# Performance work log

Measured on AMD Instinct MI355X. Metric: run time of the kernel, lower is better.

The kernel has to match this reference:

```python
import jax, jax.numpy as jnp
import numpy as np

B, T, C = 4, 2048, 2048
H, S = 32, 64
LN_EPS = 1e-5


def _layer_norm(x, w, b):
    mu = jnp.mean(x, axis=-1, keepdims=True)
    var = jnp.mean((x - mu) ** 2, axis=-1, keepdims=True)
    return (x - mu) / jnp.sqrt(var + LN_EPS) * w + b


def setup_inputs() -> dict:
    key = jax.random.key(0)
    ks = jax.random.split(key, 8)
    sc = 1.0 / np.sqrt(C)
    sc4 = 1.0 / np.sqrt(4 * C)
    return {
        "x": jax.random.normal(ks[0], (B, T, C), jnp.float32),
        "time_decay": jnp.full((H, S), -5.0, jnp.float32),
        "time_first": jnp.zeros((H, S), jnp.float32),
        "Wk": jax.random.normal(ks[1], (C, C), jnp.float32) * sc,
        "Wv": jax.random.normal(ks[2], (C, C), jnp.float32) * sc,
        "Wr": jax.random.normal(ks[3], (C, C), jnp.float32) * sc,
        "Wo": jax.random.normal(ks[4], (C, C), jnp.float32) * sc,
        "Wfk": jax.random.normal(ks[5], (C, 4 * C), jnp.float32) * sc,
        "Wfv": jax.random.normal(ks[6], (4 * C, C), jnp.float32) * sc4,
        "ln1_w": jnp.ones((C,), jnp.float32),
        "ln1_b": jnp.zeros((C,), jnp.float32),
        "ln2_w": jnp.ones((C,), jnp.float32),
        "ln2_b": jnp.zeros((C,), jnp.float32),
    }


def reference(x, time_decay, time_first, Wk, Wv, Wr, Wo, Wfk, Wfv,
              ln1_w, ln1_b, ln2_w, ln2_b):
    b, t, c = x.shape
    h, s = time_decay.shape
    xl = _layer_norm(x, ln1_w, ln1_b)
    k = (xl @ Wk).reshape(b, t, h, s)  # [B,T,H,S]
    v = (xl @ Wv).reshape(b, t, h, s)
    r = (xl @ Wr).reshape(b, t, h, s)

    decay = jnp.exp(-jnp.exp(time_decay))  # [H,S]
    u = jnp.exp(k) * v                      # [B,T,H,S]
    u_t = jnp.swapaxes(u, 0, 1)             # [T,B,H,S]

    def step(state, ut):
        state = decay * state + ut
        return state, state

    _, states = jax.lax.scan(step, jnp.zeros((b, h, s), x.dtype), u_t)  # [T,B,H,S]
    # t=0 bonus term: exp(time_first) * v_0 added to wkv only (not the state)
    states = states.at[0].add(jnp.exp(time_first) * v[:, 0])
    wkv = jnp.swapaxes(states, 0, 1)        # [B,T,H,S]

    rwkv = jax.nn.sigmoid(r) * wkv
    x = x + rwkv.reshape(b, t, c) @ Wo
    xl2 = _layer_norm(x, ln2_w, ln2_b)
    ffn = (jax.nn.relu(xl2 @ Wfk) ** 2) @ Wfv
    return x + ffn
```

## Files before the change

### kernel.cpp

```cpp
#include <hip/hip_runtime.h>
#include <hip/hip_bf16.h>
#include <stdint.h>

#define B_  4
#define T_  2048
#define C_  2048
#define H_  32
#define S_  64
#define M_  (B_ * T_)
#define C4_ (4 * C_)
#define LN_EPS 1e-5f
#define NCH 16
#define CLEN 128
#define NCHAN (B_ * C_)

typedef unsigned short u16;
typedef __attribute__((ext_vector_type(8))) short short8;
typedef __attribute__((ext_vector_type(4))) float f32x4;

__device__ __forceinline__ u16 f2bf(float f) {
  uint32_t u = __float_as_uint(f);
  u = (u + 0x7FFFu + ((u >> 16) & 1u)) >> 16;
  return (u16)u;
}
__device__ __forceinline__ float bf2f(u16 u) {
  return __uint_as_float(((uint32_t)u) << 16);
}

__device__ __forceinline__ void gload_lds16(const void* g, void* l) {
  __builtin_amdgcn_global_load_lds(
      (const __attribute__((address_space(1))) uint32_t*)g,
      (__attribute__((address_space(3))) uint32_t*)l, 16, 0, 0);
}

__global__ __launch_bounds__(256) void k_transpose_cast(
    const float* __restrict__ in, u16* __restrict__ out, int ld, int R, int Cn) {
  __shared__ float tile[32][33];
  const int tx = threadIdx.x & 31, ty = threadIdx.x >> 5;
  const int c0 = blockIdx.x * 32, r0 = blockIdx.y * 32;
#pragma unroll
  for (int i = 0; i < 4; ++i) {
    int r = ty + i * 8;
    tile[r][tx] = in[(size_t)(r0 + r) * ld + (c0 + tx)];
  }
  __syncthreads();
#pragma unroll
  for (int i = 0; i < 4; ++i) {
    int cc = ty + i * 8;
    out[(size_t)(c0 + cc) * R + (r0 + tx)] = f2bf(tile[tx][cc]);
  }
}

__global__ __launch_bounds__(256) void k_layernorm_bf16(
    const float* __restrict__ x, const float* __restrict__ w,
    const float* __restrict__ bias, u16* __restrict__ out) {
  const int row = blockIdx.x;
  const int t = threadIdx.x;
  const float* xr = x + (size_t)row * C_;
  float4 a = ((const float4*)xr)[2 * t];
  float4 b = ((const float4*)xr)[2 * t + 1];
  float s = a.x + a.y + a.z + a.w + b.x + b.y + b.z + b.w;
  float q = a.x * a.x + a.y * a.y + a.z * a.z + a.w * a.w +
            b.x * b.x + b.y * b.y + b.z * b.z + b.w * b.w;
#pragma unroll
  for (int off = 32; off > 0; off >>= 1) {
    s += __shfl_down(s, off);
    q += __shfl_down(q, off);
  }
  __shared__ float rs[8];
  const int wv = t >> 6;
  if ((t & 63) == 0) { rs[wv] = s; rs[4 + wv] = q; }
  __syncthreads();
  s = rs[0] + rs[1] + rs[2] + rs[3];
  q = rs[4] + rs[5] + rs[6] + rs[7];
  const float mean = s * (1.0f / C_);
  const float rstd = rsqrtf(q * (1.0f / C_) - mean * mean + LN_EPS);
  float4 w0 = ((const float4*)w)[2 * t], w1 = ((const float4*)w)[2 * t + 1];
  float4 b0 = ((const float4*)bias)[2 * t], b1 = ((const float4*)bias)[2 * t + 1];
  uint4 pk;
  pk.x = (uint32_t)f2bf((a.x - mean) * rstd * w0.x + b0.x) |
         ((uint32_t)f2bf((a.y - mean) * rstd * w0.y + b0.y) << 16);
  pk.y = (uint32_t)f2bf((a.z - mean) * rstd * w0.z + b0.z) |
         ((uint32_t)f2bf((a.w - mean) * rstd * w0.w + b0.w) << 16);
  pk.z = (uint32_t)f2bf((b.x - mean) * rstd * w1.x + b1.x) |
         ((uint32_t)f2bf((b.y - mean) * rstd * w1.y + b1.y) << 16);
  pk.w = (uint32_t)f2bf((b.z - mean) * rstd * w1.z + b1.z) |
         ((uint32_t)f2bf((b.w - mean) * rstd * w1.w + b1.w) << 16);
  ((uint4*)(out + (size_t)row * C_))[t] = pk;
}

__device__ __forceinline__ void stage_half(
    const u16* __restrict__ G, int ldK, int row0, int kcol0,
    u16* lds_half, int tid) {
#pragma unroll
  for (int i = 0; i < 2; ++i) {
    const int slot = i * 512 + tid;
    const int row = slot >> 2;
    const int gs = slot & 3;
    const int gsrc = gs ^ ((row >> 1) & 3);
    gload_lds16(G + (size_t)(row0 + row) * ldK + kcol0 + gsrc * 8,
                ((char*)lds_half) + i * 8192 + (tid >> 6) * 1024);
  }
}

__device__ __forceinline__ short8 frag(const u16* half_base, int row, int g0) {
  const int g = g0 ^ ((row >> 1) & 3);
  return *(const short8*)(half_base + row * 32 + g * 8);
}

template <int EPI>
__global__ __launch_bounds__(512, 2) void k_gemm8(
    const u16* __restrict__ A, const u16* __restrict__ Bt,
    void* __restrict__ Out, const float* __restrict__ Res,
    int M, int N, int K) {
  __shared__ u16 As[2][2][256 * 32];
  __shared__ u16 Bs[2][2][256 * 32];
  const int tid = threadIdx.x;
  const int wv = tid >> 6, ln = tid & 63;
  const int wm = wv >> 2, wn = wv & 3;
  const int l15 = ln & 15, g0 = ln >> 4;
  const int bm0 = blockIdx.y * 256, bn0 = blockIdx.x * 256;
  const int NT = K >> 6;

  f32x4 acc[8][4];
#pragma unroll
  for (int m = 0; m < 8; ++m)
#pragma unroll
    for (int n = 0; n < 4; ++n) acc[m][n] = (f32x4)0.0f;

  stage_half(A, K, bm0, 0, &As[0][0][0], tid);
  stage_half(Bt, K, bn0, 0, &Bs[0][0][0], tid);
  stage_half(A, K, bm0, 32, &As[0][1][0], tid);
  stage_half(Bt, K, bn0, 32, &Bs[0][1][0], tid);
  asm volatile("s_waitcnt vmcnt(4)" ::: "memory");
  __builtin_amdgcn_s_barrier();

  for (int t = 0; t < NT; ++t) {
    const int c = t & 1, nb = c ^ 1;
    const int kn = (t + 1) << 6;
    const bool stage_on = (t + 1 < NT);
    const bool lastt = (t + 1 == NT);
    short8 bfr[4], af[4];

#pragma unroll
    for (int n = 0; n < 4; ++n)
      bfr[n] = frag(&Bs[c][0][0], wn * 64 + n * 16 + l15, g0);
#pragma unroll
    for (int m = 0; m < 4; ++m)
      af[m] = frag(&As[c][0][0], wm * 128 + m * 16 + l15, g0);
    if (stage_on) stage_half(A, K, bm0, kn, &As[nb][0][0], tid);
    __builtin_amdgcn_s_barrier();
    asm volatile("s_waitcnt lgkmcnt(0)" ::: "memory");
    __builtin_amdgcn_sched_barrier(0);
    __builtin_amdgcn_s_setprio(1);
#pragma unroll
    for (int m = 0; m < 4; ++m)
#pragma unroll
      for (int n = 0; n < 4; ++n)
        acc[m][n] = __builtin_amdgcn_mfma_f32_16x16x32_bf16(af[m], bfr[n], acc[m][n], 0, 0, 0);
    __builtin_amdgcn_s_setprio(0);
    __builtin_amdgcn_sched_barrier(0);
    __builtin_amdgcn_s_barrier();

#pragma unroll
    for (int m = 0; m < 4; ++m)
      af[m] = frag(&As[c][0][0], wm * 128 + 64 + m * 16 + l15, g0);
    if (stage_on) stage_half(Bt, K, bn0, kn, &Bs[nb][0][0], tid);
    __builtin_amdgcn_s_barrier();
    asm volatile("s_waitcnt lgkmcnt(0)" ::: "memory");
    __builtin_amdgcn_sched_barrier(0);
    __builtin_amdgcn_s_setprio(1);
#pragma unroll
    for (int m = 0; m < 4; ++m)
#pragma unroll
      for (int n = 0; n < 4; ++n)
        acc[4 + m][n] = __builtin_amdgcn_mfma_f32_16x16x32_bf16(af[m], bfr[n], acc[4 + m][n], 0, 0, 0);
    __builtin_amdgcn_s_setprio(0);
    __builtin_amdgcn_sched_barrier(0);
    if (!lastt) asm volatile("s_waitcnt vmcnt(4)" ::: "memory");
    else        asm volatile("s_waitcnt vmcnt(0)" ::: "memory");
    __builtin_amdgcn_s_barrier();

#pragma unroll
    for (int n = 0; n < 4; ++n)
      bfr[n] = frag(&Bs[c][1][0], wn * 64 + n * 16 + l15, g0);
#pragma unroll
    for (int m = 0; m < 4; ++m)
      af[m] = frag(&As[c][1][0], wm * 128 + m * 16 + l15, g0);
    if (stage_on) stage_half(A, K, bm0, kn + 32, &As[nb][1][0], tid);
    __builtin_amdgcn_s_barrier();
    asm volatile("s_waitcnt lgkmcnt(0)" ::: "memory");
    __builtin_amdgcn_sched_barrier(0);
    __builtin_amdgcn_s_setprio(1);
#pragma unroll
    for (int m = 0; m < 4; ++m)
#pragma unroll
      for (int n = 0; n < 4; ++n)
        acc[m][n] = __builtin_amdgcn_mfma_f32_16x16x32_bf16(af[m], bfr[n], acc[m][n], 0, 0, 0);
    __builtin_amdgcn_s_setprio(0);
    __builtin_amdgcn_sched_barrier(0);
    __builtin_amdgcn_s_barrier();

#pragma unroll
    for (int m = 0; m < 4; ++m)
      af[m] = frag(&As[c][1][0], wm * 128 + 64 + m * 16 + l15, g0);
    if (stage_on) stage_half(Bt, K, bn0, kn + 32, &Bs[nb][1][0], tid);
    __builtin_amdgcn_s_barrier();
    asm volatile("s_waitcnt lgkmcnt(0)" ::: "memory");
    __builtin_amdgcn_sched_barrier(0);
    __builtin_amdgcn_s_setprio(1);
#pragma unroll
    for (int m = 0; m < 4; ++m)
#pragma unroll
      for (int n = 0; n < 4; ++n)
        acc[4 + m][n] = __builtin_amdgcn_mfma_f32_16x16x32_bf16(af[m], bfr[n], acc[4 + m][n], 0, 0, 0);
    __builtin_amdgcn_s_setprio(0);
    __builtin_amdgcn_sched_barrier(0);
    if (!lastt) asm volatile("s_waitcnt vmcnt(4)" ::: "memory");
    __builtin_amdgcn_s_barrier();
  }

#pragma unroll
  for (int m = 0; m < 8; ++m) {
    const int r_base = bm0 + wm * 128 + m * 16 + (ln >> 4) * 4;
#pragma unroll
    for (int n = 0; n < 4; ++n) {
      const int cidx = bn0 + wn * 64 + n * 16 + l15;
#pragma unroll
      for (int i = 0; i < 4; ++i) {
        const size_t off = (size_t)(r_base + i) * N + cidx;
        const float v = acc[m][n][i];
        if constexpr (EPI == 0) {
          ((float*)Out)[off] = v;
        } else if constexpr (EPI == 1) {
          ((float*)Out)[off] = Res[off] + v;
        } else if constexpr (EPI == 2) {
          ((u16*)Out)[off] = f2bf(v);
        } else if constexpr (EPI == 3) {
          const float tpos = v > 0.0f ? v : 0.0f;
          ((u16*)Out)[off] = f2bf(tpos * tpos);
        } else {
          ((float*)Out)[off] += v;
        }
      }
    }
  }
}

__global__ __launch_bounds__(256) void k_scan_a(
    const float* __restrict__ kk, const u16* __restrict__ vv,
    const float* __restrict__ td, float* __restrict__ Sloc) {
  const int g = blockIdx.x * 256 + threadIdx.x;
  const int j = blockIdx.y;
  const int ch = g & (C_ - 1);
  const float d = __expf(-__expf(td[ch]));
  const size_t base = ((size_t)(g >> 11) * T_ + (size_t)j * CLEN) * C_ + ch;
  float s = 0.0f;
#pragma unroll 4
  for (int t = 0; t < CLEN; ++t) {
    const size_t idx = base + (size_t)t * C_;
    s = d * s + __expf(kk[idx]) * bf2f(vv[idx]);
  }
  Sloc[(size_t)j * NCHAN + g] = s;
}

__global__ __launch_bounds__(256) void k_scan_b(
    const float* __restrict__ td, const float* __restrict__ Sloc,
    float* __restrict__ carry) {
  const int g = blockIdx.x * 256 + threadIdx.x;
  const int ch = g & (C_ - 1);
  const float dL = __expf(-__expf(td[ch]) * (float)CLEN);
  float s = 0.0f;
#pragma unroll
  for (int j = 0; j < NCH; ++j) {
    carry[(size_t)j * NCHAN + g] = s;
    s = dL * s + Sloc[(size_t)j * NCHAN + g];
  }
}

__global__ __launch_bounds__(256) void k_scan_c(
    const float* __restrict__ kk, const u16* __restrict__ vv,
    const u16* __restrict__ rr, const float* __restrict__ td,
    const float* __restrict__ tf, const float* __restrict__ carry,
    u16* __restrict__ rwkv) {
  const int g = blockIdx.x * 256 + threadIdx.x;
  const int j = blockIdx.y;
  const int ch = g & (C_ - 1);
  const float d = __expf(-__expf(td[ch]));
  const float bonus = __expf(tf[ch]);
  const size_t base = ((size_t)(g >> 11) * T_ + (size_t)j * CLEN) * C_ + ch;
  float s = carry[(size_t)j * NCHAN + g];
#pragma unroll 2
  for (int t = 0; t < CLEN; ++t) {
    const size_t idx = base + (size_t)t * C_;
    const float vval = bf2f(vv[idx]);
    s = d * s + __expf(kk[idx]) * vval;
    float wkv = s;
    if (j == 0 && t == 0) wkv += bonus * vval;
    const float rv = bf2f(rr[idx]);
    const float sg = 1.0f / (1.0f + __expf(-rv));
    rwkv[idx] = f2bf(sg * wkv);
  }
}

extern "C" void kernel_launch(void* const* d_in, const int* in_sizes, int n_in,
                              void* d_out, int out_size, void* d_ws, size_t ws_size,
                              hipStream_t stream) {
  const float* x    = (const float*)d_in[0];
  const float* td   = (const float*)d_in[1];
  const float* tf   = (const float*)d_in[2];
  const float* Wk   = (const float*)d_in[3];
  const float* Wv   = (const float*)d_in[4];
  const float* Wr   = (const float*)d_in[5];
  const float* Wo   = (const float*)d_in[6];
  const float* Wfk  = (const float*)d_in[7];
  const float* Wfv  = (const float*)d_in[8];
  const float* ln1w = (const float*)d_in[9];
  const float* ln1b = (const float*)d_in[10];
  const float* ln2w = (const float*)d_in[11];
  const float* ln2b = (const float*)d_in[12];
  float* out = (float*)d_out;

  char* p = (char*)d_ws;
  auto alloc = [&](size_t bytes) {
    char* r = p;
    p += (bytes + 255) & ~(size_t)255;
    return r;
  };
  u16*   wbuf = (u16*)alloc((size_t)C_ * C_ * 2);
  u16*   xl   = (u16*)alloc((size_t)M_ * C_ * 2);
  float* kbuf = (float*)alloc((size_t)M_ * C_ * 4);
  u16*   vbuf = (u16*)alloc((size_t)M_ * C_ * 2);
  u16*   rbuf = (u16*)alloc((size_t)M_ * C_ * 2);
  float* Sloc = (float*)alloc((size_t)NCH * NCHAN * 4);
  float* carry = (float*)alloc((size_t)NCH * NCHAN * 4);
  u16* hchunk = xl;
  u16* rwkv = rbuf;

  const dim3 tgrid(C_ / 32, C_ / 32);
  const dim3 ggrid(C_ / 256, M_ / 256);

  k_layernorm_bf16<<<M_, 256, 0, stream>>>(x, ln1w, ln1b, xl);

  k_transpose_cast<<<tgrid, 256, 0, stream>>>(Wk, wbuf, C_, C_, C_);
  k_gemm8<0><<<ggrid, 512, 0, stream>>>(xl, wbuf, kbuf, nullptr, M_, C_, C_);
  k_transpose_cast<<<tgrid, 256, 0, stream>>>(Wv, wbuf, C_, C_, C_);
  k_gemm8<2><<<ggrid, 512, 0, stream>>>(xl, wbuf, vbuf, nullptr, M_, C_, C_);
  k_transpose_cast<<<tgrid, 256, 0, stream>>>(Wr, wbuf, C_, C_, C_);
  k_gemm8<2><<<ggrid, 512, 0, stream>>>(xl, wbuf, rbuf, nullptr, M_, C_, C_);

  k_scan_a<<<dim3(NCHAN / 256, NCH), 256, 0, stream>>>(kbuf, vbuf, td, Sloc);
  k_scan_b<<<dim3(NCHAN / 256), 256, 0, stream>>>(td, Sloc, carry);
  k_scan_c<<<dim3(NCHAN / 256, NCH), 256, 0, stream>>>(kbuf, vbuf, rbuf, td, tf, carry, rwkv);

  k_transpose_cast<<<tgrid, 256, 0, stream>>>(Wo, wbuf, C_, C_, C_);
  k_gemm8<1><<<ggrid, 512, 0, stream>>>(rwkv, wbuf, out, x, M_, C_, C_);

  u16* xl2 = vbuf;
  k_layernorm_bf16<<<M_, 256, 0, stream>>>(out, ln2w, ln2b, xl2);

  for (int c = 0; c < 4; ++c) {
    k_transpose_cast<<<tgrid, 256, 0, stream>>>(Wfk + (size_t)c * C_, wbuf, C4_, C_, C_);
    k_gemm8<3><<<ggrid, 512, 0, stream>>>(xl2, wbuf, hchunk, nullptr, M_, C_, C_);
    k_transpose_cast<<<tgrid, 256, 0, stream>>>(Wfv + (size_t)c * C_ * C_, wbuf, C_, C_, C_);
    k_gemm8<4><<<ggrid, 512, 0, stream>>>(hchunk, wbuf, out, nullptr, M_, C_, C_);
  }
}
```

Baseline: 1.151 ms.

## Remap GEMM blocks per XCD, drop intra-tile barriers, halve FFN chunk count

The GEMM kernel now remaps its linear block index so that each of the eight XCDs gets a contiguous band of M rows, aiming for better L2 reuse of the shared operand tiles. The main loop is folded into a two-iteration loop, and the s_barrier calls around each MFMA group are removed, so only the per-half vmcnt barriers remain. The FFN is split into 2 chunks of width 2C instead of 4 chunks of width C. This halves the launches and the read-modify-write passes over the output, using the rbuf workspace as a larger weight buffer. Dropping barriers risks LDS races, since the next buffer is being staged while other waves may still be reading the current one.

```diff
diff --git a/kernel.cpp b/kernel.cpp
--- a/kernel.cpp
+++ b/kernel.cpp
@@ -9,6 +9,7 @@
 #define S_  64
 #define M_  (B_ * T_)
 #define C4_ (4 * C_)
+#define C2_ (2 * C_)
 #define LN_EPS 1e-5f
 #define NCH 16
 #define CLEN 128
@@ -119,7 +120,12 @@
   const int wv = tid >> 6, ln = tid & 63;
   const int wm = wv >> 2, wn = wv & 3;
   const int l15 = ln & 15, g0 = ln >> 4;
-  const int bm0 = blockIdx.y * 256, bn0 = blockIdx.x * 256;
+
+  const int lin = blockIdx.y * gridDim.x + blockIdx.x;
+  const int xcd = lin & 7, slot = lin >> 3;
+  const int bx = slot % gridDim.x;
+  const int by = xcd * (gridDim.y >> 3) + slot / gridDim.x;
+  const int bm0 = by * 256, bn0 = bx * 256;
   const int NT = K >> 6;
 
   f32x4 acc[8][4];
@@ -143,81 +149,47 @@
     short8 bfr[4], af[4];
 
 #pragma unroll
-    for (int n = 0; n < 4; ++n)
-      bfr[n] = frag(&Bs[c][0][0], wn * 64 + n * 16 + l15, g0);
-#pragma unroll
-    for (int m = 0; m < 4; ++m)
-      af[m] = frag(&As[c][0][0], wm * 128 + m * 16 + l15, g0);
-    if (stage_on) stage_half(A, K, bm0, kn, &As[nb][0][0], tid);
-    __builtin_amdgcn_s_barrier();
-    asm volatile("s_waitcnt lgkmcnt(0)" ::: "memory");
-    __builtin_amdgcn_sched_barrier(0);
-    __builtin_amdgcn_s_setprio(1);
-#pragma unroll
-    for (int m = 0; m < 4; ++m)
+    for (int h = 0; h < 2; ++h) {
 #pragma unroll
       for (int n = 0; n < 4; ++n)
-        acc[m][n] = __builtin_amdgcn_mfma_f32_16x16x32_bf16(af[m], bfr[n], acc[m][n], 0, 0, 0);
-    __builtin_amdgcn_s_setprio(0);
-    __builtin_amdgcn_sched_barrier(0);
-    __builtin_amdgcn_s_barrier();
-
-#pragma unroll
-    for (int m = 0; m < 4; ++m)
-      af[m] = frag(&As[c][0][0], wm * 128 + 64 + m * 16 + l15, g0);
-    if (stage_on) stage_half(Bt, K, bn0, kn, &Bs[nb][0][0], tid);
-    __builtin_amdgcn_s_barrier();
-    asm volatile("s_waitcnt lgkmcnt(0)" ::: "memory");
-    __builtin_amdgcn_sched_barrier(0);
-    __builtin_amdgcn_s_setprio(1);
-#pragma unroll
-    for (int m = 0; m < 4; ++m)
-#pragma unroll
-      for (int n = 0; n < 4; ++n)
-        acc[4 + m][n] = __builtin_amdgcn_mfma_f32_16x16x32_bf16(af[m], bfr[n], acc[4 + m][n], 0, 0, 0);
-    __builtin_amdgcn_s_setprio(0);
-    __builtin_amdgcn_sched_barrier(0);
-    if (!lastt) asm volatile("s_waitcnt vmcnt(4)" ::: "memory");
-    else        asm volatile("s_waitcnt vmcnt(0)" ::: "memory");
-    __builtin_amdgcn_s_barrier();
-
-#pragma unroll
-    for (int n = 0; n < 4; ++n)
-      bfr[n] = frag(&Bs[c][1][0], wn * 64 + n * 16 + l15, g0);
-#pragma unroll
-    for (int m = 0; m < 4; ++m)
-      af[m] = frag(&As[c][1][0], wm * 128 + m * 16 + l15, g0);
-    if (stage_on) stage_half(A, K, bm0, kn + 32, &As[nb][1][0], tid);
-    __builtin_amdgcn_s_barrier();
-    asm volatile("s_waitcnt lgkmcnt(0)" ::: "memory");
-    __builtin_amdgcn_sched_barrier(0);
-    __builtin_amdgcn_s_setprio(1);
-#pragma unroll
-    for (int m = 0; m < 4; ++m)
-#pragma unroll
-      for (int n = 0; n < 4; ++n)
-        acc[m][n] = __builtin_amdgcn_mfma_f32_16x16x32_bf16(af[m], bfr[n], acc[m][n], 0, 0, 0);
-    __builtin_amdgcn_s_setprio(0);
-    __builtin_amdgcn_sched_barrier(0);
-    __builtin_amdgcn_s_barrier();
-
-#pragma unroll
-    for (int m = 0; m < 4; ++m)
-      af[m] = frag(&As[c][1][0], wm * 128 + 64 + m * 16 + l15, g0);
-    if (stage_on) stage_half(Bt, K, bn0, kn + 32, &Bs[nb][1][0], tid);
-    __builtin_amdgcn_s_barrier();
-    asm volatile("s_waitcnt lgkmcnt(0)" ::: "memory");
-    __builtin_amdgcn_sched_barrier(0);
-    __builtin_amdgcn_s_setprio(1);
-#pragma unroll
-    for (int m = 0; m < 4; ++m)
-#pragma unroll
-      for (int n = 0; n < 4; ++n)
-        acc[4 + m][n] = __builtin_amdgcn_mfma_f32_16x16x32_bf16(af[m], bfr[n], acc[4 + m][n], 0, 0, 0);
-    __builtin_amdgcn_s_setprio(0);
-    __builtin_amdgcn_sched_barrier(0);
-    if (!lastt) asm volatile("s_waitcnt vmcnt(4)" ::: "memory");
-    __builtin_amdgcn_s_barrier();
+        bfr[n] = frag(&Bs[c][h][0], wn * 64 + n * 16 + l15, g0);
+#pragma unroll
+      for (int m = 0; m < 4; ++m)
+        af[m] = frag(&As[c][h][0], wm * 128 + m * 16 + l15, g0);
+      if (stage_on) stage_half(A, K, bm0, kn + h * 32, &As[nb][h][0], tid);
+      asm volatile("s_waitcnt lgkmcnt(0)" ::: "memory");
+      __builtin_amdgcn_sched_barrier(0);
+      __builtin_amdgcn_s_setprio(1);
+#pragma unroll
+      for (int m = 0; m < 4; ++m)
+#pragma unroll
+        for (int n = 0; n < 4; ++n)
+          acc[m][n] = __builtin_amdgcn_mfma_f32_16x16x32_bf16(af[m], bfr[n], acc[m][n], 0, 0, 0);
+      __builtin_amdgcn_s_setprio(0);
+
+#pragma unroll
+      for (int m = 0; m < 4; ++m)
+        af[m] = frag(&As[c][h][0], wm * 128 + 64 + m * 16 + l15, g0);
+      if (stage_on) stage_half(Bt, K, bn0, kn + h * 32, &Bs[nb][h][0], tid);
+      asm volatile("s_waitcnt lgkmcnt(0)" ::: "memory");
+      __builtin_amdgcn_sched_barrier(0);
+      __builtin_amdgcn_s_setprio(1);
+#pragma unroll
+      for (int m = 0; m < 4; ++m)
+#pragma unroll
+        for (int n = 0; n < 4; ++n)
+          acc[4 + m][n] = __builtin_amdgcn_mfma_f32_16x16x32_bf16(af[m], bfr[n], acc[4 + m][n], 0, 0, 0);
+      __builtin_amdgcn_s_setprio(0);
+
+      if (h == 0) {
+        if (!lastt) asm volatile("s_waitcnt vmcnt(4)" ::: "memory");
+        else        asm volatile("s_waitcnt vmcnt(0)" ::: "memory");
+        __builtin_amdgcn_s_barrier();
+      } else if (!lastt) {
+        asm volatile("s_waitcnt vmcnt(4)" ::: "memory");
+        __builtin_amdgcn_s_barrier();
+      }
+    }
   }
 
 #pragma unroll
@@ -334,8 +306,9 @@
   u16*   rbuf = (u16*)alloc((size_t)M_ * C_ * 2);
   float* Sloc = (float*)alloc((size_t)NCH * NCHAN * 4);
   float* carry = (float*)alloc((size_t)NCH * NCHAN * 4);
+  u16* rwkv = rbuf;
   u16* hchunk = xl;
-  u16* rwkv = rbuf;
+  u16* wfbuf = rbuf;
 
   const dim3 tgrid(C_ / 32, C_ / 32);
   const dim3 ggrid(C_ / 256, M_ / 256);
@@ -359,10 +332,14 @@
   u16* xl2 = vbuf;
   k_layernorm_bf16<<<M_, 256, 0, stream>>>(out, ln2w, ln2b, xl2);
 
-  for (int c = 0; c < 4; ++c) {
-    k_transpose_cast<<<tgrid, 256, 0, stream>>>(Wfk + (size_t)c * C_, wbuf, C4_, C_, C_);
-    k_gemm8<3><<<ggrid, 512, 0, stream>>>(xl2, wbuf, hchunk, nullptr, M_, C_, C_);
-    k_transpose_cast<<<tgrid, 256, 0, stream>>>(Wfv + (size_t)c * C_ * C_, wbuf, C_, C_, C_);
-    k_gemm8<4><<<ggrid, 512, 0, stream>>>(hchunk, wbuf, out, nullptr, M_, C_, C_);
-  }
-}
+  for (int c = 0; c < 2; ++c) {
+    k_transpose_cast<<<dim3(C2_ / 32, C_ / 32), 256, 0, stream>>>(
+        Wfk + (size_t)c * C2_, wfbuf, C4_, C_, C2_);
+    k_gemm8<3><<<dim3(C2_ / 256, M_ / 256), 512, 0, stream>>>(
+        xl2, wfbuf, hchunk, nullptr, M_, C2_, C_);
+    k_transpose_cast<<<dim3(C_ / 32, C2_ / 32), 256, 0, stream>>>(
+        Wfv + (size_t)c * C2_ * C_, wfbuf, C_, C2_, C_);
+    k_gemm8<4><<<dim3(C_ / 256, M_ / 256), 512, 0, stream>>>(
+        hchunk, wfbuf, out, nullptr, M_, C_, C2_);
+  }
+}
```

New measurement: 963.2 us. -16.3%, faster.
